# Kernel tuning notes

Hardware: AMD Instinct MI355X
Metric: run time of the kernel (lower is better)

The kernel has to match this reference:

```python
import jax, jax.numpy as jnp
import numpy as np

MAXL = 16      # max_chunk_length (hardcoded in forward)
MAXC = 1024    # max_num_chuncks (hardcoded in forward)
D = 128        # hidden_dim
SENT = 2**30   # sentinel 'end' for non-boundary positions


def setup_inputs() -> dict:
    key = jax.random.key(0)
    k1, k2, k3, k4, k5 = jax.random.split(key, 5)
    B, S = 8, 8192
    x = jax.random.normal(k1, (B, S, D), jnp.float32)
    pad_token_vector = jax.random.normal(k2, (D,), jnp.float32)
    x_ids = jax.random.randint(k3, (B, S), 0, 32000, jnp.int32)
    # end_of_seq_head params: Linear(128, 2, bias=True)
    W = jax.random.normal(k4, (D, 2), jnp.float32) * 0.1
    b = jax.random.normal(k5, (2,), jnp.float32) * 0.1
    return {"x": x, "pad_token_vector": pad_token_vector, "x_ids": x_ids,
            "pad_token_id": 0, "W": W, "b": b}


def _chunk_one(x_i, ids_i, logits_i, pad_vec, pad_id):
    # x_i: (S, D), ids_i: (S,), logits_i: (S, 2)
    S = x_i.shape[0]
    boundary = logits_i[:-1, 0] > logits_i[:-1, 1]          # (S-1,)
    pos = jnp.arange(S - 1, dtype=jnp.int32)

    # Sequential recurrence: prev_idx advances at boundaries, clipped to MAXL per chunk.
    def step(carry, inp):
        prev, cnt = carry
        bnd, ii = inp
        event = bnd & (cnt < MAXC)
        nxt = jnp.minimum(prev + MAXL, ii + 1)
        prev2 = jnp.where(event, nxt, prev)
        end = jnp.where(event, nxt, jnp.int32(SENT))
        return (prev2, cnt + event.astype(jnp.int32)), end

    (final_prev, _), ends = jax.lax.scan(
        step, (jnp.int32(0), jnp.int32(0)), (boundary, pos))
    # Chunk e consumes tokens [cum_end[e-1], cum_end[e]); ends of real events are
    # strictly increasing, sentinels sort to the back.
    ends = jnp.sort(ends)
    t = jnp.arange(S, dtype=jnp.int32)
    cid = jnp.searchsorted(ends, t, side='right').astype(jnp.int32)   # chunk id per token
    start = jnp.where(cid > 0, ends[jnp.maximum(cid - 1, 0)], 0)
    consumed = t < final_prev
    flat = jnp.where(consumed, cid * MAXL + (t - start), MAXC * MAXL)  # dump slot for pads

    # Source inits buffer to ones*pad_vec then does `+=`, so written cells = pad + x.
    buf = jnp.zeros((MAXC * MAXL + 1, D), x_i.dtype).at[flat].add(x_i)
    out = pad_vec + buf[:-1].reshape(MAXC, MAXL, D)
    idb = jnp.full((MAXC * MAXL + 1,), pad_id, jnp.float32).at[flat].set(
        ids_i.astype(jnp.float32))
    return out, idb[:-1].reshape(MAXC, MAXL)


def reference(x, pad_token_vector, x_ids, pad_token_id, W, b):
    # NOTE: source applies end_of_seq_head to the ORIGINAL x; the 2 transformer
    # blocks write x_chunking which is never used (dead code) -> omitted.
    logits = x @ W + b                                       # (B, S, 2)
    f = lambda xi, ii, li: _chunk_one(xi, ii, li, pad_token_vector, pad_token_id)
    output_tensor, output_token_ids = jax.vmap(f)(x, x_ids, logits)
    return output_tensor, output_token_ids
```

## Files before the change

kernel.cpp:

```cpp
#include <hip/hip_runtime.h>
#include <hip/hip_bf16.h>
#include <climits>

#define S 8192
#define D_DIM 128
#define MAXL 16
#define MAXC 1024
#define NB 8

__global__ __launch_bounds__(256) void bnd_kernel(
    const float* __restrict__ x, const float* __restrict__ W,
    const float* __restrict__ bias, unsigned char* __restrict__ bnd) {
  int wid = (blockIdx.x * blockDim.x + threadIdx.x) >> 6;
  int lane = threadIdx.x & 63;
  if (wid >= NB * (S - 1)) return;
  int b = wid / (S - 1);
  int t = wid % (S - 1);
  const float* xr = x + ((size_t)(b * S + t)) * D_DIM;
  float2 xv = *(const float2*)(xr + lane * 2);
  float2 wA = *(const float2*)(W + lane * 4);
  float2 wB = *(const float2*)(W + lane * 4 + 2);
  double d0 = (double)xv.x * wA.x + (double)xv.y * wB.x;
  double d1 = (double)xv.x * wA.y + (double)xv.y * wB.y;
  for (int off = 32; off; off >>= 1) {
    d0 += __shfl_down(d0, off, 64);
    d1 += __shfl_down(d1, off, 64);
  }
  if (lane == 0) {
    bnd[b * S + t] = ((d0 + (double)bias[0]) > (d1 + (double)bias[1])) ? 1 : 0;
  }
}

__global__ __launch_bounds__(1024) void scan_kernel(
    const unsigned char* __restrict__ bnd, int* __restrict__ ends,
    int* __restrict__ numEv) {
  int b = blockIdx.x;
  int tid = threadIdx.x;
  __shared__ int sc[1024];
  __shared__ int evpos[1024];
  __shared__ int sm[1024];

  const unsigned char* bb = bnd + b * S;
  unsigned long long w = *(const unsigned long long*)(bb + tid * 8);
  int flags[8];
  int cnt = 0;
#pragma unroll
  for (int i = 0; i < 8; ++i) {
    int p = tid * 8 + i;
    int f = (p < S - 1) ? (int)((w >> (8 * i)) & 1ull) : 0;
    flags[i] = f;
    cnt += f;
  }
  sc[tid] = cnt;
  __syncthreads();
  for (int off = 1; off < 1024; off <<= 1) {
    int v = sc[tid];
    int add = (tid >= off) ? sc[tid - off] : 0;
    __syncthreads();
    sc[tid] = v + add;
    __syncthreads();
  }
  int total = sc[1023];
  int idx = sc[tid] - cnt;
#pragma unroll
  for (int i = 0; i < 8; ++i) {
    if (flags[i]) {
      if (idx < MAXC) evpos[idx] = tid * 8 + i;
      idx++;
    }
  }
  __syncthreads();
  int nev = total < MAXC ? total : MAXC;
  int g = (tid < nev) ? (evpos[tid] + 1 - MAXL * tid) : INT_MAX;
  sm[tid] = g;
  __syncthreads();
  for (int off = 1; off < 1024; off <<= 1) {
    int v = sm[tid];
    int m = (tid >= off) ? sm[tid - off] : INT_MAX;
    __syncthreads();
    sm[tid] = v < m ? v : m;
    __syncthreads();
  }
  if (tid < nev) {
    int mk = sm[tid];
    int cap = mk < MAXL ? mk : MAXL;
    ends[b * MAXC + tid] = MAXL * tid + cap;
  }
  if (tid == 0) numEv[b] = nev;
}

__global__ __launch_bounds__(256) void out_kernel(
    const float* __restrict__ x, const float* __restrict__ pad,
    const int* __restrict__ xids, const int* __restrict__ pad_id,
    const int* __restrict__ ends, const int* __restrict__ numEv,
    float* __restrict__ out_t, float* __restrict__ out_ids) {
  int gid = blockIdx.x * 256 + threadIdx.x;
  int row = gid >> 5;
  int q = gid & 31;
  int b = row >> 14;
  int rem = row & 16383;
  int c = rem >> 4;
  int l = rem & 15;
  int nev = numEv[b];
  int tok = -1;
  if (c < nev) {
    int e = ends[b * MAXC + c];
    int s = c ? ends[b * MAXC + c - 1] : 0;
    if (l < e - s) tok = s + l;
  }
  float4 o = ((const float4*)pad)[q];
  if (tok >= 0) {
    float4 xv = ((const float4*)(x + ((size_t)(b * S + tok)) * D_DIM))[q];
    o.x += xv.x; o.y += xv.y; o.z += xv.z; o.w += xv.w;
  }
  ((float4*)out_t)[(size_t)row * 32 + q] = o;
  if (q == 0) {
    out_ids[row] = (tok >= 0) ? (float)xids[b * S + tok] : (float)(*pad_id);
  }
}

extern "C" void kernel_launch(void* const* d_in, const int* in_sizes, int n_in,
                              void* d_out, int out_size, void* d_ws, size_t ws_size,
                              hipStream_t stream) {
  const float* x = (const float*)d_in[0];
  const float* pad_vec = (const float*)d_in[1];
  const int* x_ids = (const int*)d_in[2];
  const int* pad_id = (const int*)d_in[3];
  const float* W = (const float*)d_in[4];
  const float* bias = (const float*)d_in[5];

  unsigned char* bnd = (unsigned char*)d_ws;
  int* ends = (int*)((char*)d_ws + NB * S);
  int* numEv = (int*)((char*)d_ws + NB * S + NB * MAXC * 4);

  float* out_t = (float*)d_out;
  float* out_ids = out_t + (size_t)NB * MAXC * MAXL * D_DIM;

  int rows = NB * (S - 1);
  int blocksA = (rows * 64 + 255) / 256;
  hipLaunchKernelGGL(bnd_kernel, dim3(blocksA), dim3(256), 0, stream,
                     x, W, bias, bnd);

  hipLaunchKernelGGL(scan_kernel, dim3(NB), dim3(1024), 0, stream,
                     bnd, ends, numEv);

  int out_rows = NB * MAXC * MAXL;
  int blocksC = out_rows / 8;
  hipLaunchKernelGGL(out_kernel, dim3(blocksC), dim3(256), 0, stream,
                     x, pad_vec, x_ids, pad_id, ends, numEv, out_t, out_ids);
}
```

Baseline: 125.3 us.

## Process four rows per wave in boundary kernel and use wave-level scans

The boundary kernel now assigns 16 lanes per row, four rows per wavefront, using float4 loads. It also folds the two logits into a single difference dot product against a bias threshold, which cuts the shuffle reductions from two to one. The scan kernel replaces its 1024-wide shared-memory Hillis-Steele scans, which needed many block barriers, with wave-level shuffle scans plus a small cross-wave step, and counts flags with a popcount. Computing the logit difference in double could change rounding in near-tie boundary cases.

```diff
diff --git a/kernel.cpp b/kernel.cpp
--- a/kernel.cpp
+++ b/kernel.cpp
@@ -11,23 +11,39 @@
 __global__ __launch_bounds__(256) void bnd_kernel(
     const float* __restrict__ x, const float* __restrict__ W,
     const float* __restrict__ bias, unsigned char* __restrict__ bnd) {
-  int wid = (blockIdx.x * blockDim.x + threadIdx.x) >> 6;
+  int gtid = blockIdx.x * 256 + threadIdx.x;
+  int wid = gtid >> 6;
   int lane = threadIdx.x & 63;
-  if (wid >= NB * (S - 1)) return;
-  int b = wid / (S - 1);
-  int t = wid % (S - 1);
-  const float* xr = x + ((size_t)(b * S + t)) * D_DIM;
-  float2 xv = *(const float2*)(xr + lane * 2);
-  float2 wA = *(const float2*)(W + lane * 4);
-  float2 wB = *(const float2*)(W + lane * 4 + 2);
-  double d0 = (double)xv.x * wA.x + (double)xv.y * wB.x;
-  double d1 = (double)xv.x * wA.y + (double)xv.y * wB.y;
-  for (int off = 32; off; off >>= 1) {
-    d0 += __shfl_down(d0, off, 64);
-    d1 += __shfl_down(d1, off, 64);
+  int sub = lane >> 4;
+  int fg = lane & 15;
+  int row = wid * 4 + sub;
+  bool valid = row < NB * (S - 1);
+  double d = 0.0;
+  int b = 0, t = 0;
+  if (valid) {
+    b = row / (S - 1);
+    t = row - b * (S - 1);
+    const float* xr = x + ((size_t)b * S + t) * D_DIM + fg * 8;
+    float4 xa = ((const float4*)xr)[0];
+    float4 xb = ((const float4*)xr)[1];
+    const float* wr = W + fg * 16;
+    float4 w0 = ((const float4*)wr)[0];
+    float4 w1 = ((const float4*)wr)[1];
+    float4 w2 = ((const float4*)wr)[2];
+    float4 w3 = ((const float4*)wr)[3];
+    d += (double)xa.x * ((double)w0.x - (double)w0.y);
+    d += (double)xa.y * ((double)w0.z - (double)w0.w);
+    d += (double)xa.z * ((double)w1.x - (double)w1.y);
+    d += (double)xa.w * ((double)w1.z - (double)w1.w);
+    d += (double)xb.x * ((double)w2.x - (double)w2.y);
+    d += (double)xb.y * ((double)w2.z - (double)w2.w);
+    d += (double)xb.z * ((double)w3.x - (double)w3.y);
+    d += (double)xb.w * ((double)w3.z - (double)w3.w);
   }
-  if (lane == 0) {
-    bnd[b * S + t] = ((d0 + (double)bias[0]) > (d1 + (double)bias[1])) ? 1 : 0;
+  for (int m = 1; m < 16; m <<= 1) d += __shfl_xor(d, m, 64);
+  if (valid && fg == 0) {
+    double thr = (double)bias[1] - (double)bias[0];
+    bnd[b * S + t] = (d > thr) ? 1 : 0;
   }
 }
 
@@ -36,54 +52,75 @@
     int* __restrict__ numEv) {
   int b = blockIdx.x;
   int tid = threadIdx.x;
-  __shared__ int sc[1024];
+  int lane = tid & 63;
+  int wv = tid >> 6;
+  __shared__ int wsum[16];
+  __shared__ int wmin[16];
   __shared__ int evpos[1024];
-  __shared__ int sm[1024];
+  __shared__ int s_total;
 
   const unsigned char* bb = bnd + b * S;
   unsigned long long w = *(const unsigned long long*)(bb + tid * 8);
-  int flags[8];
-  int cnt = 0;
+  if (tid == 1023) w &= 0x00FFFFFFFFFFFFFFull;
+  unsigned long long bits = w & 0x0101010101010101ull;
+  int cnt = __popcll(bits);
+
+  int inc = cnt;
+  for (int off = 1; off < 64; off <<= 1) {
+    int v = __shfl_up(inc, off, 64);
+    if (lane >= off) inc += v;
+  }
+  if (lane == 63) wsum[wv] = inc;
+  __syncthreads();
+  if (wv == 0 && lane < 16) {
+    int v = wsum[lane];
+    int iv = v;
+    for (int off = 1; off < 16; off <<= 1) {
+      int u = __shfl_up(iv, off, 64);
+      if (lane >= off) iv += u;
+    }
+    if (lane == 15) s_total = iv;
+    wsum[lane] = iv - v;
+  }
+  __syncthreads();
+  int excl = wsum[wv] + inc - cnt;
+
+  int idx = excl;
 #pragma unroll
   for (int i = 0; i < 8; ++i) {
-    int p = tid * 8 + i;
-    int f = (p < S - 1) ? (int)((w >> (8 * i)) & 1ull) : 0;
-    flags[i] = f;
-    cnt += f;
-  }
-  sc[tid] = cnt;
-  __syncthreads();
-  for (int off = 1; off < 1024; off <<= 1) {
-    int v = sc[tid];
-    int add = (tid >= off) ? sc[tid - off] : 0;
-    __syncthreads();
-    sc[tid] = v + add;
-    __syncthreads();
-  }
-  int total = sc[1023];
-  int idx = sc[tid] - cnt;
-#pragma unroll
-  for (int i = 0; i < 8; ++i) {
-    if (flags[i]) {
+    if ((w >> (8 * i)) & 1ull) {
       if (idx < MAXC) evpos[idx] = tid * 8 + i;
       idx++;
     }
   }
   __syncthreads();
+  int total = s_total;
   int nev = total < MAXC ? total : MAXC;
+
   int g = (tid < nev) ? (evpos[tid] + 1 - MAXL * tid) : INT_MAX;
-  sm[tid] = g;
+  int incm = g;
+  for (int off = 1; off < 64; off <<= 1) {
+    int v = __shfl_up(incm, off, 64);
+    if (lane >= off) incm = incm < v ? incm : v;
+  }
+  if (lane == 63) wmin[wv] = incm;
   __syncthreads();
-  for (int off = 1; off < 1024; off <<= 1) {
-    int v = sm[tid];
-    int m = (tid >= off) ? sm[tid - off] : INT_MAX;
-    __syncthreads();
-    sm[tid] = v < m ? v : m;
-    __syncthreads();
+  if (wv == 0 && lane < 16) {
+    int iv = wmin[lane];
+    for (int off = 1; off < 16; off <<= 1) {
+      int u = __shfl_up(iv, off, 64);
+      if (lane >= off) iv = iv < u ? iv : u;
+    }
+    int ex = __shfl_up(iv, 1, 64);
+    if (lane == 0) ex = INT_MAX;
+    wmin[lane] = ex;
   }
+  __syncthreads();
+  int wex = wmin[wv];
+  int m = incm < wex ? incm : wex;
+
   if (tid < nev) {
-    int mk = sm[tid];
-    int cap = mk < MAXL ? mk : MAXL;
+    int cap = m < MAXL ? m : MAXL;
     ends[b * MAXC + tid] = MAXL * tid + cap;
   }
   if (tid == 0) numEv[b] = nev;
@@ -137,7 +174,8 @@
   float* out_ids = out_t + (size_t)NB * MAXC * MAXL * D_DIM;
 
   int rows = NB * (S - 1);
-  int blocksA = (rows * 64 + 255) / 256;
+  int waves = (rows + 3) / 4;
+  int blocksA = (waves * 64 + 255) / 256;
   hipLaunchKernelGGL(bnd_kernel, dim3(blocksA), dim3(256), 0, stream,
                      x, W, bias, bnd);
 
```

Measured after the change: 112.5 us (median of 2 runs). 1.11x faster.
